# Kernel tuning notes

Hardware: AMD Instinct MI355X
Metric: run time of the kernel (lower is better)

## Reference

```python
import jax, jax.numpy as jnp
import numpy as np

B, D, H = 64, 2048, 2048


def setup_inputs() -> dict:
    key = jax.random.key(0)
    ks = jax.random.split(key, 10)
    s = 1.0 / np.sqrt(D)  # Linear init scale
    # small z scale keeps exp() gates in a sane range
    return {
        "t": jnp.zeros((), jnp.float32),
        "z": jax.random.normal(ks[0], (B, D), jnp.float32) * 0.02,
        "K": jax.random.normal(ks[1], (B, D), jnp.float32) * 0.02,
        "V": jax.random.normal(ks[2], (B, D, D), jnp.float32) * 0.02,
        "Wq": jax.random.normal(ks[3], (D, D), jnp.float32) * s,
        "bq": jnp.zeros((D,), jnp.float32),
        "Wk": jax.random.normal(ks[4], (D, D), jnp.float32) * s,
        "bk": jnp.zeros((D,), jnp.float32),
        "Wv": jax.random.normal(ks[5], (D, D), jnp.float32) * s,
        "bv": jnp.zeros((D,), jnp.float32),
        "W1": jax.random.normal(ks[6], (D, H), jnp.float32) * s,
        "b1": jnp.zeros((H,), jnp.float32),
        "W2": jax.random.normal(ks[7], (H, D), jnp.float32) * (1.0 / np.sqrt(H)),
        "b2": jnp.zeros((D,), jnp.float32),
    }


def reference(t, z, K, V, Wq, bq, Wk, bk, Wv, bv, W1, b1, W2, b2):
    # get_ode_gradient_nn: 2-layer tanh MLP (stand-in for user ode_func_net)
    dz = jnp.tanh(z @ W1 + b1) @ W2 + b2                 # [B, D]
    dK = jnp.exp(z @ Wk + bk)                            # exp gate, [B, D]
    v = z @ Wv + bv                                      # [B, D]
    dV = jnp.einsum("bd,be->bde", v, dK)                # rank-1 outer update, [B, D, D]
    q = jnp.exp(z @ Wq + bq)                             # [B, D]
    a = jnp.sum(q * dK, axis=-1, keepdims=True)          # q . dK, [B, 1]
    dq = q * (dz @ Wq + bq)                              # [B, D]
    da = a + jnp.sum(dq * K, axis=-1, keepdims=True)     # [B, 1]
    dc = jnp.einsum("bde,be->bd", dV, q) + jnp.einsum("bde,be->bd", V, dq)  # [B, D]
    return (dz, da, dc, dK, dV)
```

## Files before the change

### kernel.cpp

```cpp
#include <hip/hip_runtime.h>
#include <cstddef>
#include <math.h>

#define BB 64
#define DD 2048
#define HH 2048
#define BD (BB*DD)

template<int MT>
__device__ __forceinline__ void gemm_body(
    const float* __restrict__ A0, const float* __restrict__ A1,
    const float* __restrict__ W, float* __restrict__ part, int kc)
{
    constexpr int KC = 32;
    constexpr int RT = MT / 16;
    __shared__ float As[KC][MT];
    __shared__ float Ws[KC][64];

    const int t  = threadIdx.x;
    const int n0 = blockIdx.x * 64;
    const int k0 = blockIdx.y * kc;
    const int i  = t >> 4;
    const int j  = t & 15;

    float acc[RT][4];
#pragma unroll
    for (int r = 0; r < RT; ++r)
#pragma unroll
        for (int c = 0; c < 4; ++c) acc[r][c] = 0.f;

    for (int kk0 = 0; kk0 < kc; kk0 += KC) {
        {
            int kk = t >> 3;
            int nn = (t & 7) << 3;
            const float* s = W + (size_t)(k0 + kk0 + kk) * DD + n0 + nn;
            *(float4*)&Ws[kk][nn]     = *(const float4*)s;
            *(float4*)&Ws[kk][nn + 4] = *(const float4*)(s + 4);
        }
        if constexpr (MT == 64) {
            int m  = t & 63;
            int kb = (t >> 6) << 3;
            const float* s = A0 + (size_t)m * DD + k0 + kk0 + kb;
            float4 a0 = *(const float4*)s;
            float4 a1 = *(const float4*)(s + 4);
            As[kb+0][m] = a0.x; As[kb+1][m] = a0.y;
            As[kb+2][m] = a0.z; As[kb+3][m] = a0.w;
            As[kb+4][m] = a1.x; As[kb+5][m] = a1.y;
            As[kb+6][m] = a1.z; As[kb+7][m] = a1.w;
        } else {
            int m  = t & 127;
            int kb = (t >> 7) << 4;
            const float* base = (m < 64) ? (A0 + (size_t)m * DD)
                                         : (A1 + (size_t)(m - 64) * DD);
            const float* s = base + k0 + kk0 + kb;
#pragma unroll
            for (int p = 0; p < 4; ++p) {
                float4 av = *(const float4*)(s + p * 4);
                As[kb+p*4+0][m] = av.x; As[kb+p*4+1][m] = av.y;
                As[kb+p*4+2][m] = av.z; As[kb+p*4+3][m] = av.w;
            }
        }
        __syncthreads();

#pragma unroll
        for (int kk = 0; kk < KC; ++kk) {
            float4 wv = *(float4*)&Ws[kk][j << 2];
#pragma unroll
            for (int rq = 0; rq < RT / 4; ++rq) {
                float4 av = *(float4*)&As[kk][i * RT + rq * 4];
                acc[rq*4+0][0] = fmaf(av.x, wv.x, acc[rq*4+0][0]);
                acc[rq*4+0][1] = fmaf(av.x, wv.y, acc[rq*4+0][1]);
                acc[rq*4+0][2] = fmaf(av.x, wv.z, acc[rq*4+0][2]);
                acc[rq*4+0][3] = fmaf(av.x, wv.w, acc[rq*4+0][3]);
                acc[rq*4+1][0] = fmaf(av.y, wv.x, acc[rq*4+1][0]);
                acc[rq*4+1][1] = fmaf(av.y, wv.y, acc[rq*4+1][1]);
                acc[rq*4+1][2] = fmaf(av.y, wv.z, acc[rq*4+1][2]);
                acc[rq*4+1][3] = fmaf(av.y, wv.w, acc[rq*4+1][3]);
                acc[rq*4+2][0] = fmaf(av.z, wv.x, acc[rq*4+2][0]);
                acc[rq*4+2][1] = fmaf(av.z, wv.y, acc[rq*4+2][1]);
                acc[rq*4+2][2] = fmaf(av.z, wv.z, acc[rq*4+2][2]);
                acc[rq*4+2][3] = fmaf(av.z, wv.w, acc[rq*4+2][3]);
                acc[rq*4+3][0] = fmaf(av.w, wv.x, acc[rq*4+3][0]);
                acc[rq*4+3][1] = fmaf(av.w, wv.y, acc[rq*4+3][1]);
                acc[rq*4+3][2] = fmaf(av.w, wv.z, acc[rq*4+3][2]);
                acc[rq*4+3][3] = fmaf(av.w, wv.w, acc[rq*4+3][3]);
            }
        }
        __syncthreads();
    }

    float* P = part + (size_t)blockIdx.y * MT * DD + n0 + (j << 2);
#pragma unroll
    for (int r = 0; r < RT; ++r) {
        *(float4*)&P[(size_t)(i * RT + r) * DD] =
            make_float4(acc[r][0], acc[r][1], acc[r][2], acc[r][3]);
    }
}

__global__ __launch_bounds__(256) void gemm64(
    const float* __restrict__ A, const float* __restrict__ W,
    float* __restrict__ part, int kc)
{
    gemm_body<64>(A, A, W, part, kc);
}

__global__ __launch_bounds__(256) void gemm64_z2(
    const float* __restrict__ A,
    const float* __restrict__ W0, const float* __restrict__ W1,
    float* __restrict__ p0, float* __restrict__ p1, int kc)
{
    const float* W = blockIdx.z ? W1 : W0;
    float*       P = blockIdx.z ? p1 : p0;
    gemm_body<64>(A, A, W, P, kc);
}

__global__ __launch_bounds__(256) void gemm128(
    const float* __restrict__ A0, const float* __restrict__ A1,
    const float* __restrict__ W, float* __restrict__ part, int kc)
{
    gemm_body<128>(A0, A1, W, part, kc);
}

__global__ __launch_bounds__(256) void epilogue(
    const float* __restrict__ part, const float* __restrict__ bias,
    float* __restrict__ out, int act, int KS)
{
    int idx = blockIdx.x * 256 + threadIdx.x;
    float s = bias[idx & (DD - 1)];
    for (int ks = 0; ks < KS; ++ks) s += part[(size_t)ks * BD + idx];
    if (act == 1) s = tanhf(s);
    out[idx] = s;
}

__global__ __launch_bounds__(256) void epilogue_kv(
    const float* __restrict__ pk, const float* __restrict__ pv,
    const float* __restrict__ bk, const float* __restrict__ bv,
    float* __restrict__ dKo, float* __restrict__ vo, int KS)
{
    int idx = blockIdx.x * 256 + threadIdx.x;
    int d = idx & (DD - 1);
    float sk = 0.f, sv = 0.f;
    for (int ks = 0; ks < KS; ++ks) {
        sk += pk[(size_t)ks * BD + idx];
        sv += pv[(size_t)ks * BD + idx];
    }
    dKo[idx] = expf(sk + bk[d]);
    vo[idx]  = sv + bv[d];
}

__global__ __launch_bounds__(256) void epilogue_q_dq(
    const float* __restrict__ pq, const float* __restrict__ bq,
    float* __restrict__ qo, float* __restrict__ dqo, int KS)
{
    int idx = blockIdx.x * 256 + threadIdx.x;
    int b = idx >> 11, d = idx & (DD - 1);
    float sq = 0.f, sd = 0.f;
    for (int ks = 0; ks < KS; ++ks) {
        const float* P = pq + (size_t)ks * (128 * DD);
        sq += P[(size_t)b * DD + d];
        sd += P[(size_t)(b + 64) * DD + d];
    }
    float bb = bq[d];
    float qv = expf(sq + bb);
    qo[idx]  = qv;
    dqo[idx] = qv * (sd + bb);
}

__global__ __launch_bounds__(256) void reduce_a_da(
    const float* __restrict__ q, const float* __restrict__ dK,
    const float* __restrict__ dq, const float* __restrict__ Kin,
    float* __restrict__ a_ws, float* __restrict__ da_out)
{
    int b = blockIdx.x;
    int t = threadIdx.x;
    const float* qb  = q   + (size_t)b * DD;
    const float* dKb = dK  + (size_t)b * DD;
    const float* dqb = dq  + (size_t)b * DD;
    const float* Kb  = Kin + (size_t)b * DD;

    float s1 = 0.f, s2 = 0.f;
    for (int i = t; i < DD; i += 256) {
        s1 = fmaf(qb[i],  dKb[i], s1);
        s2 = fmaf(dqb[i], Kb[i],  s2);
    }
#pragma unroll
    for (int off = 32; off; off >>= 1) {
        s1 += __shfl_down(s1, off);
        s2 += __shfl_down(s2, off);
    }
    __shared__ float r1[4], r2[4];
    if ((t & 63) == 0) { r1[t >> 6] = s1; r2[t >> 6] = s2; }
    __syncthreads();
    if (t == 0) {
        float a  = r1[0] + r1[1] + r1[2] + r1[3];
        float k2 = r2[0] + r2[1] + r2[2] + r2[3];
        a_ws[b]   = a;
        da_out[b] = a + k2;
    }
}

__global__ __launch_bounds__(256) void fused_dv_dc(
    const float* __restrict__ V, const float* __restrict__ v,
    const float* __restrict__ dK, const float* __restrict__ dq,
    const float* __restrict__ a, float* __restrict__ dV,
    float* __restrict__ dc)
{
    int b     = blockIdx.x >> 5;
    int chunk = blockIdx.x & 31;
    int wave  = threadIdx.x >> 6;
    int lane  = threadIdx.x & 63;

    const float4* dK4 = (const float4*)(dK + ((size_t)b << 11));
    const float4* dq4 = (const float4*)(dq + ((size_t)b << 11));
    float4 dKr[8], dqr[8];
#pragma unroll
    for (int u = 0; u < 8; ++u) {
        dKr[u] = dK4[u * 64 + lane];
        dqr[u] = dq4[u * 64 + lane];
    }
    float ab = a[b];

    int row0 = chunk * 64 + wave * 16;
    for (int rr = 0; rr < 16; ++rr) {
        int row = row0 + rr;
        size_t off = ((size_t)((b << 11) | row)) << 11;
        const float4* V4  = (const float4*)(V  + off);
        float4*       dV4 = (float4*)(dV + off);

        float dot = 0.f;
        float vr = v[((size_t)b << 11) + row];
#pragma unroll
        for (int u = 0; u < 8; ++u) {
            float4 Vv = V4[u * 64 + lane];
            dot += Vv.x * dqr[u].x + Vv.y * dqr[u].y
                 + Vv.z * dqr[u].z + Vv.w * dqr[u].w;
        }
#pragma unroll
        for (int u = 0; u < 8; ++u) {
            float4 o;
            o.x = vr * dKr[u].x; o.y = vr * dKr[u].y;
            o.z = vr * dKr[u].z; o.w = vr * dKr[u].w;
            dV4[u * 64 + lane] = o;
        }
#pragma unroll
        for (int s = 32; s; s >>= 1) dot += __shfl_down(dot, s);
        if (lane == 0) dc[((size_t)b << 11) + row] = vr * ab + dot;
    }
}

extern "C" void kernel_launch(void* const* d_in, const int* in_sizes, int n_in,
                              void* d_out, int out_size, void* d_ws, size_t ws_size,
                              hipStream_t stream)
{
    const float* z   = (const float*)d_in[1];
    const float* Kin = (const float*)d_in[2];
    const float* Vin = (const float*)d_in[3];
    const float* Wq  = (const float*)d_in[4];
    const float* bq  = (const float*)d_in[5];
    const float* Wk  = (const float*)d_in[6];
    const float* bk  = (const float*)d_in[7];
    const float* Wv  = (const float*)d_in[8];
    const float* bv  = (const float*)d_in[9];
    const float* W1  = (const float*)d_in[10];
    const float* b1  = (const float*)d_in[11];
    const float* W2  = (const float*)d_in[12];
    const float* b2  = (const float*)d_in[13];

    float* out   = (float*)d_out;
    float* o_dz  = out;
    float* o_da  = out + BD;
    float* o_dc  = out + BD + BB;
    float* o_dK  = out + 2 * BD + BB;
    float* o_dV  = out + 3 * BD + BB;

    float* ws    = (float*)d_ws;
    float* ws_h  = ws;
    float* ws_v  = ws + BD;
    float* ws_q  = ws + 2 * BD;
    float* ws_dq = ws + 3 * BD;
    float* ws_a  = ws + 4 * BD;
    float* pool  = ws + 4 * BD + 64;

    int KS = 16;
    while (KS > 1 &&
           ((size_t)(4 * BD + 64) + 2ull * KS * BD) * 4ull > ws_size)
        KS >>= 1;
    int kc = DD / KS;

    float* p0 = pool;
    float* p1 = pool + (size_t)KS * BD;

    dim3 blk(256);
    dim3 gG(DD / 64, KS);
    dim3 gG2(DD / 64, KS, 2);
    dim3 gE(BD / 256);

    gemm64<<<gG, blk, 0, stream>>>(z, W1, p0, kc);
    epilogue<<<gE, blk, 0, stream>>>(p0, b1, ws_h, 1, KS);

    gemm64<<<gG, blk, 0, stream>>>(ws_h, W2, p0, kc);
    epilogue<<<gE, blk, 0, stream>>>(p0, b2, o_dz, 0, KS);

    gemm64_z2<<<gG2, blk, 0, stream>>>(z, Wk, Wv, p0, p1, kc);
    epilogue_kv<<<gE, blk, 0, stream>>>(p0, p1, bk, bv, o_dK, ws_v, KS);

    gemm128<<<gG, blk, 0, stream>>>(z, o_dz, Wq, p0, kc);
    epilogue_q_dq<<<gE, blk, 0, stream>>>(p0, bq, ws_q, ws_dq, KS);

    reduce_a_da<<<dim3(BB), blk, 0, stream>>>(ws_q, o_dK, ws_dq, Kin, ws_a, o_da);

    fused_dv_dc<<<dim3(BB * 32), blk, 0, stream>>>(Vin, ws_v, o_dK, ws_dq, ws_a,
                                                   o_dV, o_dc);
}
```

Measured before the change: 513.2 us.

## Run projection GEMMs on bf16 MFMA with per-call weight transpose-conversion

Adds kernels that convert and transpose the five weight matrices and z to bf16 on every call, then computes all five projection GEMMs with 16x16x32 bf16 MFMA instructions using direct global-to-LDS loads and split-K partial sums. The fp32 FMA GEMM path stays as a fallback when the workspace is too small. The dV/dc kernel is restructured to handle four rows per group and uses nontemporal loads and stores for the large V read and dV write. The intent is to replace slow scalar fp32 GEMMs with matrix cores, at the cost of an extra weight-conversion pass each call and reduced precision in the inputs.

```diff
diff --git a/kernel.cpp b/kernel.cpp
--- a/kernel.cpp
+++ b/kernel.cpp
@@ -6,9 +6,209 @@
 #define DD 2048
 #define HH 2048
 #define BD (BB*DD)
+#define WN (2048*2048)
+
+typedef unsigned short u16;
+typedef __attribute__((ext_vector_type(8))) short bf16x8;
+typedef __attribute__((ext_vector_type(4))) float f32x4;
+typedef __attribute__((ext_vector_type(4))) float f4;
+
+__device__ __forceinline__ u16 f2b(float x) {
+    union { float f; unsigned u; } v; v.f = x;
+    unsigned r = v.u + 0x7FFFu + ((v.u >> 16) & 1u);
+    return (u16)(r >> 16);
+}
+
+__device__ __forceinline__ void gload16(const void* g, void* l) {
+    __builtin_amdgcn_global_load_lds(
+        (__attribute__((address_space(1))) void*)g,
+        (__attribute__((address_space(3))) void*)l, 16, 0, 0);
+}
+
+
+__global__ __launch_bounds__(256) void wconv(
+    const float* __restrict__ W0, const float* __restrict__ W1,
+    const float* __restrict__ W2, const float* __restrict__ W3,
+    const float* __restrict__ W4, u16* __restrict__ wt)
+{
+    const float* W;
+    switch (blockIdx.z) {
+        case 0: W = W0; break; case 1: W = W1; break;
+        case 2: W = W2; break; case 3: W = W3; break;
+        default: W = W4; break;
+    }
+    u16* T = wt + (size_t)blockIdx.z * WN;
+
+    __shared__ u16 tile[64][66];
+    int k0 = blockIdx.x * 64, n0 = blockIdx.y * 64;
+    int t = threadIdx.x;
+    {
+        int r = t >> 2, c0 = (t & 3) * 16;
+        const float* src = W + (size_t)(k0 + r) * DD + n0 + c0;
+#pragma unroll
+        for (int q = 0; q < 4; ++q) {
+            float4 f = *(const float4*)(src + q * 4);
+            tile[r][c0 + q*4 + 0] = f2b(f.x);
+            tile[r][c0 + q*4 + 1] = f2b(f.y);
+            tile[r][c0 + q*4 + 2] = f2b(f.z);
+            tile[r][c0 + q*4 + 3] = f2b(f.w);
+        }
+    }
+    __syncthreads();
+    {
+        int rn = t >> 2, ck = (t & 3) * 16;
+        u16 o[16];
+#pragma unroll
+        for (int j = 0; j < 16; ++j) o[j] = tile[ck + j][rn];
+        u16* dst = T + (size_t)(n0 + rn) * DD + k0 + ck;
+        *(bf16x8*)dst       = *(bf16x8*)&o[0];
+        *(bf16x8*)(dst + 8) = *(bf16x8*)&o[8];
+    }
+}
+
+__global__ __launch_bounds__(256) void zconv(
+    const float* __restrict__ z, u16* __restrict__ zb)
+{
+    int i = (blockIdx.x * 256 + threadIdx.x) * 4;
+    float4 f = *(const float4*)&z[i];
+    union { u16 u[4]; uint2 v; } o;
+    o.u[0] = f2b(f.x); o.u[1] = f2b(f.y); o.u[2] = f2b(f.z); o.u[3] = f2b(f.w);
+    *(uint2*)&zb[i] = o.v;
+}
+
+__device__ __forceinline__ void gemm_bf16_body(
+    const u16* __restrict__ A, const u16* __restrict__ Wt,
+    float* __restrict__ P, int kc)
+{
+    __shared__ u16 Als[64 * 32];
+    __shared__ u16 Wls[64 * 32];
+    const int t = threadIdx.x, w = t >> 6, lane = t & 63;
+    const int n0 = blockIdx.x * 64;
+    const int k0 = blockIdx.y * kc;
+
+    f32x4 acc[4];
+#pragma unroll
+    for (int mt = 0; mt < 4; ++mt) acc[mt] = (f32x4){0.f, 0.f, 0.f, 0.f};
+
+    const int srow = lane >> 2;
+    const int sk   = (lane & 3) * 8;
+    const u16* gA = A  + (size_t)(w * 16 + srow) * DD + k0 + sk;
+    const u16* gW = Wt + (size_t)(n0 + w * 16 + srow) * DD + k0 + sk;
+    u16* lA = &Als[w * 512];
+    u16* lW = &Wls[w * 512];
+
+    const int lane15 = lane & 15;
+    const int k8 = (lane >> 4) * 8;
+
+    for (int kk = 0; kk < kc; kk += 32) {
+        gload16(gA, lA);
+        gload16(gW, lW);
+        gA += 32; gW += 32;
+        __syncthreads();
+
+        bf16x8 bfrag = *(const bf16x8*)&Wls[(w * 16 + lane15) * 32 + k8];
+#pragma unroll
+        for (int mt = 0; mt < 4; ++mt) {
+            bf16x8 afrag = *(const bf16x8*)&Als[(mt * 16 + lane15) * 32 + k8];
+            acc[mt] = __builtin_amdgcn_mfma_f32_16x16x32_bf16(
+                afrag, bfrag, acc[mt], 0, 0, 0);
+        }
+        __syncthreads();
+    }
+
+    const int col = n0 + w * 16 + lane15;
+    const int r4 = (lane >> 4) * 4;
+#pragma unroll
+    for (int mt = 0; mt < 4; ++mt)
+#pragma unroll
+        for (int j = 0; j < 4; ++j)
+            P[(size_t)(mt * 16 + r4 + j) * DD + col] = acc[mt][j];
+}
+
+__global__ __launch_bounds__(256) void gemm_bf16_single(
+    const u16* __restrict__ A, const u16* __restrict__ Wt,
+    float* __restrict__ part, int kc)
+{
+    float* P = part + (size_t)blockIdx.y * 64 * DD;
+    gemm_bf16_body(A, Wt, P, kc);
+}
+
+__global__ __launch_bounds__(256) void gemm_bf16_kv(
+    const u16* __restrict__ A, const u16* __restrict__ Wkt,
+    const u16* __restrict__ Wvt, float* __restrict__ p0,
+    float* __restrict__ p1, int kc)
+{
+    const u16* Wt = blockIdx.z ? Wvt : Wkt;
+    float* P = (blockIdx.z ? p1 : p0) + (size_t)blockIdx.y * 64 * DD;
+    gemm_bf16_body(A, Wt, P, kc);
+}
+
+__global__ __launch_bounds__(256) void gemm_bf16_q(
+    const u16* __restrict__ zb, const u16* __restrict__ dzb,
+    const u16* __restrict__ Wqt, float* __restrict__ part, int kc)
+{
+    const u16* A = blockIdx.z ? dzb : zb;
+    float* P = part + ((size_t)blockIdx.y * 128 + blockIdx.z * 64) * DD;
+    gemm_bf16_body(A, Wqt, P, kc);
+}
+
+__global__ __launch_bounds__(256) void ep_h(
+    const float* __restrict__ p, const float* __restrict__ b1,
+    u16* __restrict__ hb, int KS)
+{
+    int i = blockIdx.x * 256 + threadIdx.x;
+    float s = b1[i & (DD - 1)];
+    for (int ks = 0; ks < KS; ++ks) s += p[(size_t)ks * BD + i];
+    hb[i] = f2b(tanhf(s));
+}
+
+__global__ __launch_bounds__(256) void ep_dz(
+    const float* __restrict__ p, const float* __restrict__ b2,
+    float* __restrict__ dz, u16* __restrict__ dzb, int KS)
+{
+    int i = blockIdx.x * 256 + threadIdx.x;
+    float s = b2[i & (DD - 1)];
+    for (int ks = 0; ks < KS; ++ks) s += p[(size_t)ks * BD + i];
+    dz[i]  = s;
+    dzb[i] = f2b(s);
+}
+
+__global__ __launch_bounds__(256) void ep_kv(
+    const float* __restrict__ pk, const float* __restrict__ pv,
+    const float* __restrict__ bk, const float* __restrict__ bv,
+    float* __restrict__ dKo, float* __restrict__ vo, int KS)
+{
+    int i = blockIdx.x * 256 + threadIdx.x;
+    int d = i & (DD - 1);
+    float sk = 0.f, sv = 0.f;
+    for (int ks = 0; ks < KS; ++ks) {
+        sk += pk[(size_t)ks * BD + i];
+        sv += pv[(size_t)ks * BD + i];
+    }
+    dKo[i] = expf(sk + bk[d]);
+    vo[i]  = sv + bv[d];
+}
+
+__global__ __launch_bounds__(256) void ep_q_dq(
+    const float* __restrict__ pq, const float* __restrict__ bq,
+    float* __restrict__ qo, float* __restrict__ dqo, int KS)
+{
+    int i = blockIdx.x * 256 + threadIdx.x;
+    int b = i >> 11, d = i & (DD - 1);
+    float sq = 0.f, sd = 0.f;
+    for (int ks = 0; ks < KS; ++ks) {
+        const float* P = pq + (size_t)ks * (128 * DD);
+        sq += P[(size_t)b * DD + d];
+        sd += P[(size_t)(b + 64) * DD + d];
+    }
+    float bb = bq[d];
+    float qv = expf(sq + bb);
+    qo[i]  = qv;
+    dqo[i] = qv * (sd + bb);
+}
 
 template<int MT>
-__device__ __forceinline__ void gemm_body(
+__device__ __forceinline__ void gemm_body_f32(
     const float* __restrict__ A0, const float* __restrict__ A1,
     const float* __restrict__ W, float* __restrict__ part, int kc)
 {
@@ -61,7 +261,6 @@
             }
         }
         __syncthreads();
-
 #pragma unroll
         for (int kk = 0; kk < KC; ++kk) {
             float4 wv = *(float4*)&Ws[kk][j << 2];
@@ -91,18 +290,15 @@
 
     float* P = part + (size_t)blockIdx.y * MT * DD + n0 + (j << 2);
 #pragma unroll
-    for (int r = 0; r < RT; ++r) {
+    for (int r = 0; r < RT; ++r)
         *(float4*)&P[(size_t)(i * RT + r) * DD] =
             make_float4(acc[r][0], acc[r][1], acc[r][2], acc[r][3]);
-    }
 }
 
 __global__ __launch_bounds__(256) void gemm64(
     const float* __restrict__ A, const float* __restrict__ W,
     float* __restrict__ part, int kc)
-{
-    gemm_body<64>(A, A, W, part, kc);
-}
+{ gemm_body_f32<64>(A, A, W, part, kc); }
 
 __global__ __launch_bounds__(256) void gemm64_z2(
     const float* __restrict__ A,
@@ -111,59 +307,23 @@
 {
     const float* W = blockIdx.z ? W1 : W0;
     float*       P = blockIdx.z ? p1 : p0;
-    gemm_body<64>(A, A, W, P, kc);
+    gemm_body_f32<64>(A, A, W, P, kc);
 }
 
 __global__ __launch_bounds__(256) void gemm128(
     const float* __restrict__ A0, const float* __restrict__ A1,
     const float* __restrict__ W, float* __restrict__ part, int kc)
-{
-    gemm_body<128>(A0, A1, W, part, kc);
-}
-
-__global__ __launch_bounds__(256) void epilogue(
+{ gemm_body_f32<128>(A0, A1, W, part, kc); }
+
+__global__ __launch_bounds__(256) void epilogue_f32(
     const float* __restrict__ part, const float* __restrict__ bias,
     float* __restrict__ out, int act, int KS)
 {
-    int idx = blockIdx.x * 256 + threadIdx.x;
-    float s = bias[idx & (DD - 1)];
-    for (int ks = 0; ks < KS; ++ks) s += part[(size_t)ks * BD + idx];
+    int i = blockIdx.x * 256 + threadIdx.x;
+    float s = bias[i & (DD - 1)];
+    for (int ks = 0; ks < KS; ++ks) s += part[(size_t)ks * BD + i];
     if (act == 1) s = tanhf(s);
-    out[idx] = s;
-}
-
-__global__ __launch_bounds__(256) void epilogue_kv(
-    const float* __restrict__ pk, const float* __restrict__ pv,
-    const float* __restrict__ bk, const float* __restrict__ bv,
-    float* __restrict__ dKo, float* __restrict__ vo, int KS)
-{
-    int idx = blockIdx.x * 256 + threadIdx.x;
-    int d = idx & (DD - 1);
-    float sk = 0.f, sv = 0.f;
-    for (int ks = 0; ks < KS; ++ks) {
-        sk += pk[(size_t)ks * BD + idx];
-        sv += pv[(size_t)ks * BD + idx];
-    }
-    dKo[idx] = expf(sk + bk[d]);
-    vo[idx]  = sv + bv[d];
-}
-
-__global__ __launch_bounds__(256) void epilogue_q_dq(
-    const float* __restrict__ pq, const float* __restrict__ bq,
-    float* __restrict__ qo, float* __restrict__ dqo, int KS)
-{
-    int idx = blockIdx.x * 256 + threadIdx.x;
-    int b = idx >> 11, d = idx & (DD - 1);
-    float sq = 0.f, sd = 0.f;
-    for (int ks = 0; ks < KS; ++ks) {
-        const float* P = pq + (size_t)ks * (128 * DD);
-        sq += P[(size_t)b * DD + d];
-        sd += P[(size_t)(b + 64) * DD + d];
-    }
-    float bb = bq[d];
-    float qv = expf(sq + bb);
-    qo[idx]  = qv;
-    dqo[idx] = qv * (sd + bb);
+    out[i] = s;
 }
 
 __global__ __launch_bounds__(256) void reduce_a_da(
@@ -210,41 +370,48 @@
     int wave  = threadIdx.x >> 6;
     int lane  = threadIdx.x & 63;
 
-    const float4* dK4 = (const float4*)(dK + ((size_t)b << 11));
-    const float4* dq4 = (const float4*)(dq + ((size_t)b << 11));
-    float4 dKr[8], dqr[8];
+    const f4* dK4 = (const f4*)(dK + ((size_t)b << 11));
+    const f4* dq4 = (const f4*)(dq + ((size_t)b << 11));
+    f4 dKr[8], dqr[8];
 #pragma unroll
     for (int u = 0; u < 8; ++u) {
         dKr[u] = dK4[u * 64 + lane];
         dqr[u] = dq4[u * 64 + lane];
     }
     float ab = a[b];
-
     int row0 = chunk * 64 + wave * 16;
-    for (int rr = 0; rr < 16; ++rr) {
-        int row = row0 + rr;
-        size_t off = ((size_t)((b << 11) | row)) << 11;
-        const float4* V4  = (const float4*)(V  + off);
-        float4*       dV4 = (float4*)(dV + off);
-
-        float dot = 0.f;
-        float vr = v[((size_t)b << 11) + row];
-#pragma unroll
-        for (int u = 0; u < 8; ++u) {
-            float4 Vv = V4[u * 64 + lane];
-            dot += Vv.x * dqr[u].x + Vv.y * dqr[u].y
-                 + Vv.z * dqr[u].z + Vv.w * dqr[u].w;
-        }
-#pragma unroll
-        for (int u = 0; u < 8; ++u) {
-            float4 o;
-            o.x = vr * dKr[u].x; o.y = vr * dKr[u].y;
-            o.z = vr * dKr[u].z; o.w = vr * dKr[u].w;
-            dV4[u * 64 + lane] = o;
-        }
-#pragma unroll
-        for (int s = 32; s; s >>= 1) dot += __shfl_down(dot, s);
-        if (lane == 0) dc[((size_t)b << 11) + row] = vr * ab + dot;
+
+    for (int g = 0; g < 4; ++g) {
+        float dot[4];
+#pragma unroll
+        for (int r2 = 0; r2 < 4; ++r2) {
+            int row = row0 + g * 4 + r2;
+            size_t off = ((size_t)((b << 11) | row)) << 11;
+            const f4* V4  = (const f4*)(V  + off);
+            f4*       dV4 = (f4*)(dV + off);
+            float vr = v[((size_t)b << 11) + row];
+            float d  = 0.f;
+#pragma unroll
+            for (int u = 0; u < 8; ++u) {
+                f4 Vv = __builtin_nontemporal_load(&V4[u * 64 + lane]);
+                d += Vv[0] * dqr[u][0] + Vv[1] * dqr[u][1]
+                   + Vv[2] * dqr[u][2] + Vv[3] * dqr[u][3];
+                f4 o = vr * dKr[u];
+                __builtin_nontemporal_store(o, &dV4[u * 64 + lane]);
+            }
+            dot[r2] = d;
+        }
+#pragma unroll
+        for (int r2 = 0; r2 < 4; ++r2) {
+            float d = dot[r2];
+#pragma unroll
+            for (int s = 32; s; s >>= 1) d += __shfl_down(d, s);
+            if (lane == 0) {
+                int row = row0 + g * 4 + r2;
+                dc[((size_t)b << 11) + row] =
+                    v[((size_t)b << 11) + row] * ab + d;
+            }
+        }
     }
 }
 
@@ -274,38 +441,80 @@
     float* o_dV  = out + 3 * BD + BB;
 
     float* ws    = (float*)d_ws;
-    float* ws_h  = ws;
-    float* ws_v  = ws + BD;
-    float* ws_q  = ws + 2 * BD;
-    float* ws_dq = ws + 3 * BD;
-    float* ws_a  = ws + 4 * BD;
-    float* pool  = ws + 4 * BD + 64;
-
-    int KS = 16;
-    while (KS > 1 &&
-           ((size_t)(4 * BD + 64) + 2ull * KS * BD) * 4ull > ws_size)
-        KS >>= 1;
-    int kc = DD / KS;
-
-    float* p0 = pool;
-    float* p1 = pool + (size_t)KS * BD;
+    float* ws_v  = ws;
+    float* ws_q  = ws + BD;
+    float* ws_dq = ws + 2 * BD;
+    float* ws_a  = ws + 3 * BD;
+    float* ws_h  = ws + 3 * BD + 64;
+    u16*   zb    = (u16*)(ws + 4 * BD + 64);
+    u16*   hb    = zb + BD;
+    u16*   dzb   = hb + BD;
+    u16*   wt    = dzb + BD;
+    float* poolb = (float*)(wt + 5ull * WN);
+
+    const size_t pre_fl = 4ull * BD + 64 + (3ull * BD + 5ull * WN) / 2;
+
+    int KS = 0;
+    for (int ks = 16; ks >= 4; ks >>= 1)
+        if ((pre_fl + 2ull * ks * BD) * 4ull <= ws_size) { KS = ks; break; }
 
     dim3 blk(256);
-    dim3 gG(DD / 64, KS);
-    dim3 gG2(DD / 64, KS, 2);
     dim3 gE(BD / 256);
 
-    gemm64<<<gG, blk, 0, stream>>>(z, W1, p0, kc);
-    epilogue<<<gE, blk, 0, stream>>>(p0, b1, ws_h, 1, KS);
-
-    gemm64<<<gG, blk, 0, stream>>>(ws_h, W2, p0, kc);
-    epilogue<<<gE, blk, 0, stream>>>(p0, b2, o_dz, 0, KS);
-
-    gemm64_z2<<<gG2, blk, 0, stream>>>(z, Wk, Wv, p0, p1, kc);
-    epilogue_kv<<<gE, blk, 0, stream>>>(p0, p1, bk, bv, o_dK, ws_v, KS);
-
-    gemm128<<<gG, blk, 0, stream>>>(z, o_dz, Wq, p0, kc);
-    epilogue_q_dq<<<gE, blk, 0, stream>>>(p0, bq, ws_q, ws_dq, KS);
+    if (KS) {
+        int kc = DD / KS;
+        float* p0 = poolb;
+        float* p1 = poolb + (size_t)KS * BD;
+
+        dim3 gW(32, 32, 5);
+        dim3 gG(32, KS);
+        dim3 gG2(32, KS, 2);
+
+        wconv<<<gW, blk, 0, stream>>>(W1, W2, Wk, Wv, Wq, wt);
+        zconv<<<dim3(BD / 1024), blk, 0, stream>>>(z, zb);
+
+        u16* W1t = wt;
+        u16* W2t = wt + 1ull * WN;
+        u16* Wkt = wt + 2ull * WN;
+        u16* Wvt = wt + 3ull * WN;
+        u16* Wqt = wt + 4ull * WN;
+
+        gemm_bf16_single<<<gG, blk, 0, stream>>>(zb, W1t, p0, kc);
+        ep_h<<<gE, blk, 0, stream>>>(p0, b1, hb, KS);
+
+        gemm_bf16_single<<<gG, blk, 0, stream>>>(hb, W2t, p0, kc);
+        ep_dz<<<gE, blk, 0, stream>>>(p0, b2, o_dz, dzb, KS);
+
+        gemm_bf16_kv<<<gG2, blk, 0, stream>>>(zb, Wkt, Wvt, p0, p1, kc);
+        ep_kv<<<gE, blk, 0, stream>>>(p0, p1, bk, bv, o_dK, ws_v, KS);
+
+        gemm_bf16_q<<<gG2, blk, 0, stream>>>(zb, dzb, Wqt, p0, kc);
+        ep_q_dq<<<gE, blk, 0, stream>>>(p0, bq, ws_q, ws_dq, KS);
+    } else {
+        float* pool = ws + 4 * BD + 64;
+        int KSf = 16;
+        while (KSf > 1 &&
+               ((size_t)(4 * BD + 64) + 2ull * KSf * BD) * 4ull > ws_size)
+            KSf >>= 1;
+        int kc = DD / KSf;
+        float* p0 = pool;
+        float* p1 = pool + (size_t)KSf * BD;
+
+        dim3 gG(DD / 64, KSf);
+        dim3 gG2(DD / 64, KSf, 2);
+
+        gemm64<<<gG, blk, 0, stream>>>(z, W1, p0, kc);
+        epilogue_f32<<<gE, blk, 0, stream>>>(p0, b1, ws_h, 1, KSf);
+
+        gemm64<<<gG, blk, 0, stream>>>(ws_h, W2, p0, kc);
+        epilogue_f32<<<gE, blk, 0, stream>>>(p0, b2, o_dz, 0, KSf);
+
+        gemm64_z2<<<gG2, blk, 0, stream>>>(z, Wk, Wv, p0, p1, kc);
+        ep_kv<<<gE, blk, 0, stream>>>(p0, p1, bk, bv, o_dK, ws_v, KSf);
+
+        gemm128<<<gG, blk, 0, stream>>>(z, o_dz, Wq, p0, kc);
+        ep_q_dq<<<gE, blk, 0, stream>>>(p0, bq, ws_q, ws_dq, KSf);
+    }
 
     reduce_a_da<<<dim3(BB), blk, 0, stream>>>(ws_q, o_dK, ws_dq, Kin, ws_a, o_da);
 
```

New measurement: 493.9 us. 1.04x faster.
